# Kernel tuning notes

Measured on AMD Instinct MI355X. Metric: run time of the kernel, lower is better.

Reference implementation:

```python
import jax, jax.numpy as jnp
import numpy as np

_EPS = 1e-4  # pytorch3d se3_exp_map clamps the SQUARED rotation angle at this eps


def _hat(w):
    # w: [..., 3] -> skew-symmetric [..., 3, 3]
    wx, wy, wz = w[..., 0], w[..., 1], w[..., 2]
    z = jnp.zeros_like(wx)
    return jnp.stack([
        jnp.stack([z, -wz, wy], axis=-1),
        jnp.stack([wz, z, -wx], axis=-1),
        jnp.stack([-wy, wx, z], axis=-1),
    ], axis=-2)


def _se3_exp(dofs):
    # dofs: [..., 6] = (log_translation, log_rotation), pytorch3d convention.
    # Returns R [..., 3, 3] and t [..., 3] such that p' = R @ p + t,
    # matching pytorch3d's row-convention matrix M ([:3,:3]=R^T, [3,:3]=t)
    # applied as p' = p @ M[:3,:3] + M[3,:3].
    t_log = dofs[..., :3]
    w = dofs[..., 3:]
    nrms = jnp.sum(w * w, axis=-1)
    theta = jnp.sqrt(jnp.clip(nrms, _EPS))  # [...]
    H = _hat(w)
    H2 = H @ H
    st, ct = jnp.sin(theta), jnp.cos(theta)
    f1 = (st / theta)[..., None, None]
    f2 = ((1.0 - ct) / (theta * theta))[..., None, None]
    f3 = ((theta - st) / (theta * theta * theta))[..., None, None]
    I = jnp.eye(3, dtype=dofs.dtype)
    R = I + f1 * H + f2 * H2            # Rodrigues
    V = I + f2 * H + f3 * H2            # left-Jacobian of SO(3)
    t = jnp.einsum('...ij,...j->...i', V, t_log)
    return R, t


def setup_inputs() -> dict:
    key = jax.random.key(0)
    k1, k2 = jax.random.split(key)
    B, T, N = 64, 28, 4096
    X_v = jax.random.normal(k1, (B, T, N, 3), dtype=jnp.float32)
    dofs = jax.random.normal(k2, (B, T, 6), dtype=jnp.float32)
    return {"X_v": X_v, "dofs": dofs}


def reference(X_v, dofs):
    # Fused, fully-batched version of the per-tooth python loop:
    # one SE3 exp over all (B,T) transforms + one batched point transform.
    R, t = _se3_exp(dofs)                                  # [B,T,3,3], [B,T,3]
    out = jnp.einsum('btij,btnj->btni', R, X_v) + t[:, :, None, :]
    return out
```

## Files before the change

kernel.cpp:

```cpp
#include <hip/hip_runtime.h>


__global__ __launch_bounds__(256) void se3_apply_kernel(
    const float* __restrict__ X,
    const float* __restrict__ dofs,
    float* __restrict__ out,
    int n3,
    int tilesPerBT)
{
    __shared__ float lds[3072];

    const int bt   = blockIdx.x / tilesPerBT;
    const int tile = blockIdx.x - bt * tilesPerBT;
    const int t    = threadIdx.x;

    const long long baseF = (long long)bt * (long long)n3 + (long long)tile * 3072;
    const int f4InBT   = tile * 768;
    const int n4       = n3 >> 2;
    const float4* __restrict__ Xp = (const float4*)(X + baseF);
    float4* __restrict__ Op       = (float4*)(out + baseF);
    float4* lds4 = (float4*)lds;

    float4 v0, v1, v2;
    const bool g0 = (f4InBT + t        ) < n4;
    const bool g1 = (f4InBT + t + 256  ) < n4;
    const bool g2 = (f4InBT + t + 512  ) < n4;
    if (g0) v0 = Xp[t];
    if (g1) v1 = Xp[t + 256];
    if (g2) v2 = Xp[t + 512];

    const float* d = dofs + bt * 6;
    const float tx = d[0], ty = d[1], tz = d[2];
    const float wx = d[3], wy = d[4], wz = d[5];

    const float nrm2  = wx * wx + wy * wy + wz * wz;
    const float th2   = fmaxf(nrm2, 1e-4f);
    const float theta = sqrtf(th2);
    const float st = sinf(theta);
    const float ct = cosf(theta);
    const float f1 = st / theta;
    const float f2 = (1.0f - ct) / th2;
    const float f3 = (theta - st) / (th2 * theta);

    const float xx = wx * wx, yy = wy * wy, zz = wz * wz;
    const float xy = wx * wy, xz = wx * wz, yz = wy * wz;

    const float R00 = 1.0f - f2 * (yy + zz);
    const float R01 = f2 * xy - f1 * wz;
    const float R02 = f2 * xz + f1 * wy;
    const float R10 = f2 * xy + f1 * wz;
    const float R11 = 1.0f - f2 * (xx + zz);
    const float R12 = f2 * yz - f1 * wx;
    const float R20 = f2 * xz - f1 * wy;
    const float R21 = f2 * yz + f1 * wx;
    const float R22 = 1.0f - f2 * (xx + yy);

    const float V00 = 1.0f - f3 * (yy + zz);
    const float V01 = f3 * xy - f2 * wz;
    const float V02 = f3 * xz + f2 * wy;
    const float V10 = f3 * xy + f2 * wz;
    const float V11 = 1.0f - f3 * (xx + zz);
    const float V12 = f3 * yz - f2 * wx;
    const float V20 = f3 * xz - f2 * wy;
    const float V21 = f3 * yz + f2 * wx;
    const float V22 = 1.0f - f3 * (xx + yy);

    const float Tx = V00 * tx + V01 * ty + V02 * tz;
    const float Ty = V10 * tx + V11 * ty + V12 * tz;
    const float Tz = V20 * tx + V21 * ty + V22 * tz;

    if (g0) lds4[t]       = v0;
    if (g1) lds4[t + 256] = v1;
    if (g2) lds4[t + 512] = v2;
    __syncthreads();

#pragma unroll
    for (int j = 0; j < 4; ++j) {
        const int p = 3 * (t + 256 * j);
        const float px = lds[p + 0];
        const float py = lds[p + 1];
        const float pz = lds[p + 2];
        lds[p + 0] = fmaf(R00, px, fmaf(R01, py, fmaf(R02, pz, Tx)));
        lds[p + 1] = fmaf(R10, px, fmaf(R11, py, fmaf(R12, pz, Ty)));
        lds[p + 2] = fmaf(R20, px, fmaf(R21, py, fmaf(R22, pz, Tz)));
    }
    __syncthreads();

    if (g0) Op[t]       = lds4[t];
    if (g1) Op[t + 256] = lds4[t + 256];
    if (g2) Op[t + 512] = lds4[t + 512];
}

extern "C" void kernel_launch(void* const* d_in, const int* in_sizes, int n_in,
                              void* d_out, int out_size, void* d_ws, size_t ws_size,
                              hipStream_t stream) {
    const float* X    = (const float*)d_in[0];
    const float* dofs = (const float*)d_in[1];
    float* out        = (float*)d_out;

    const int BT = in_sizes[1] / 6;
    const int n3 = in_sizes[0] / BT;

    const int tilesPerBT = (n3 + 3071) / 3072;

    dim3 grid((unsigned)(BT * tilesPerBT));
    se3_apply_kernel<<<grid, 256, 0, stream>>>(X, dofs, out, n3, tilesPerBT);
}
```

Measured before the change: 156.9 us.

## Process one BT per block with per-wave chunk loop and register prefetch

Launches one block per (b,t) transform, computing the SE3 exp once per block instead of once per tile. Each wave owns a private LDS slice and loops over chunks, prefetching the next chunk into registers while transforming the current one. Block-wide barriers are replaced by wave-local LDS waitcnt fences. The cost is fewer blocks and fewer outstanding loads per wave, which may reduce memory-level parallelism.

```diff
diff --git a/kernel.cpp b/kernel.cpp
--- a/kernel.cpp
+++ b/kernel.cpp
@@ -1,33 +1,19 @@
 #include <hip/hip_runtime.h>
 
+
+#define LDS_FENCE() asm volatile("s_waitcnt lgkmcnt(0)" ::: "memory")
 
 __global__ __launch_bounds__(256) void se3_apply_kernel(
     const float* __restrict__ X,
     const float* __restrict__ dofs,
     float* __restrict__ out,
-    int n3,
-    int tilesPerBT)
+    int n3)
 {
     __shared__ float lds[3072];
 
-    const int bt   = blockIdx.x / tilesPerBT;
-    const int tile = blockIdx.x - bt * tilesPerBT;
-    const int t    = threadIdx.x;
-
-    const long long baseF = (long long)bt * (long long)n3 + (long long)tile * 3072;
-    const int f4InBT   = tile * 768;
-    const int n4       = n3 >> 2;
-    const float4* __restrict__ Xp = (const float4*)(X + baseF);
-    float4* __restrict__ Op       = (float4*)(out + baseF);
-    float4* lds4 = (float4*)lds;
-
-    float4 v0, v1, v2;
-    const bool g0 = (f4InBT + t        ) < n4;
-    const bool g1 = (f4InBT + t + 256  ) < n4;
-    const bool g2 = (f4InBT + t + 512  ) < n4;
-    if (g0) v0 = Xp[t];
-    if (g1) v1 = Xp[t + 256];
-    if (g2) v2 = Xp[t + 512];
+    const int bt   = blockIdx.x;
+    const int lane = threadIdx.x & 63;
+    const int w    = threadIdx.x >> 6;
 
     const float* d = dofs + bt * 6;
     const float tx = d[0], ty = d[1], tz = d[2];
@@ -69,26 +55,68 @@
     const float Ty = V10 * tx + V11 * ty + V12 * tz;
     const float Tz = V20 * tx + V21 * ty + V22 * tz;
 
-    if (g0) lds4[t]       = v0;
-    if (g1) lds4[t + 256] = v1;
-    if (g2) lds4[t + 512] = v2;
-    __syncthreads();
+    const long long btBase = (long long)bt * (long long)n3;
+    float* const wlds   = lds + w * 768;
+    float4* const wlds4 = (float4*)wlds;
+
+    const int nChunks = n3 / 768;
+
+    float4 v0, v1, v2;
+    {
+        const float4* __restrict__ g4 = (const float4*)(X + btBase + (long long)w * 768);
+        v0 = g4[lane];
+        v1 = g4[lane + 64];
+        v2 = g4[lane + 128];
+    }
+
+    for (int c = w; c < nChunks; c += 4) {
+        const long long base = btBase + (long long)c * 768;
+        float4* __restrict__ o4 = (float4*)(out + base);
+
+        wlds4[lane]       = v0;
+        wlds4[lane + 64]  = v1;
+        wlds4[lane + 128] = v2;
+        LDS_FENCE();
+
+        const int cn = c + 4;
+        if (cn < nChunks) {
+            const float4* __restrict__ gn = (const float4*)(X + btBase + (long long)cn * 768);
+            v0 = gn[lane];
+            v1 = gn[lane + 64];
+            v2 = gn[lane + 128];
+        }
 
 #pragma unroll
-    for (int j = 0; j < 4; ++j) {
-        const int p = 3 * (t + 256 * j);
-        const float px = lds[p + 0];
-        const float py = lds[p + 1];
-        const float pz = lds[p + 2];
-        lds[p + 0] = fmaf(R00, px, fmaf(R01, py, fmaf(R02, pz, Tx)));
-        lds[p + 1] = fmaf(R10, px, fmaf(R11, py, fmaf(R12, pz, Ty)));
-        lds[p + 2] = fmaf(R20, px, fmaf(R21, py, fmaf(R22, pz, Tz)));
+        for (int j = 0; j < 4; ++j) {
+            const int p = 3 * (lane + 64 * j);
+            const float px = wlds[p + 0];
+            const float py = wlds[p + 1];
+            const float pz = wlds[p + 2];
+            wlds[p + 0] = fmaf(R00, px, fmaf(R01, py, fmaf(R02, pz, Tx)));
+            wlds[p + 1] = fmaf(R10, px, fmaf(R11, py, fmaf(R12, pz, Ty)));
+            wlds[p + 2] = fmaf(R20, px, fmaf(R21, py, fmaf(R22, pz, Tz)));
+        }
+        LDS_FENCE();
+
+        o4[lane]       = wlds4[lane];
+        o4[lane + 64]  = wlds4[lane + 64];
+        o4[lane + 128] = wlds4[lane + 128];
+        LDS_FENCE();
     }
-    __syncthreads();
 
-    if (g0) Op[t]       = lds4[t];
-    if (g1) Op[t + 256] = lds4[t + 256];
-    if (g2) Op[t + 512] = lds4[t + 512];
+    const int tailF = n3 - nChunks * 768;
+    if (tailF > 0 && w == 0) {
+        const int tailPts = tailF / 3;
+        const long long tbase = btBase + (long long)nChunks * 768;
+        for (int p = lane; p < tailPts; p += 64) {
+            const float px = X[tbase + 3 * p + 0];
+            const float py = X[tbase + 3 * p + 1];
+            const float pz = X[tbase + 3 * p + 2];
+            out[tbase + 3 * p + 0] = fmaf(R00, px, fmaf(R01, py, fmaf(R02, pz, Tx)));
+            out[tbase + 3 * p + 1] = fmaf(R10, px, fmaf(R11, py, fmaf(R12, pz, Ty)));
+            out[tbase + 3 * p + 2] = fmaf(R20, px, fmaf(R21, py, fmaf(R22, pz, Tz)));
+        }
+    }
 }
 
 extern "C" void kernel_launch(void* const* d_in, const int* in_sizes, int n_in,
@@ -101,8 +129,6 @@
     const int BT = in_sizes[1] / 6;
     const int n3 = in_sizes[0] / BT;
 
-    const int tilesPerBT = (n3 + 3071) / 3072;
-
-    dim3 grid((unsigned)(BT * tilesPerBT));
-    se3_apply_kernel<<<grid, 256, 0, stream>>>(X, dofs, out, n3, tilesPerBT);
+    dim3 grid((unsigned)BT);
+    se3_apply_kernel<<<grid, 256, 0, stream>>>(X, dofs, out, n3);
 }
```

After: 158.9 us. Within noise of the previous version (+1.3%).
